# Kernel tuning notes

Measured on AMD Instinct MI355X. Metric: run time of the kernel, lower is better.

The kernel has to match this reference:

```python
import jax, jax.numpy as jnp
import numpy as np

N_NODES = 50000   # num graph nodes
N_EDGES = 800000  # avg degree 16
D = 96            # in_channels == out_channels (residual aggr_out + x)


def setup_inputs() -> dict:
    key = jax.random.key(0)
    k0, k1, k2, k3, k4 = jax.random.split(key, 5)
    x = jax.random.normal(k0, (N_NODES, D), dtype=jnp.float32)
    edge_index = jax.random.randint(k1, (2, N_EDGES), 0, N_NODES)  # [2,E]: row0=src(j), row1=dst(i)
    edge_weight = jax.random.uniform(k2, (N_EDGES,), dtype=jnp.float32)
    pagerank = jax.random.uniform(k3, (N_NODES,), dtype=jnp.float32)
    # nn.Linear(in_channels, out_channels) params
    W = jax.random.normal(k4, (D, D), dtype=jnp.float32) / np.sqrt(D).astype(np.float32)
    b = jnp.zeros((D,), dtype=jnp.float32)
    return {"x": x, "edge_index": edge_index, "edge_weight": edge_weight,
            "pagerank": pagerank, "W": W, "b": b}


def reference(x, edge_index, edge_weight, pagerank, W, b):
    # CGCConv (PyG MessagePassing, aggr='add', flow source_to_target):
    #   message: edge_weight * x_j * pagerank_j   (gather from source nodes)
    #   aggregate: scatter-add to destination nodes
    #   update: Linear(aggr_out + x)
    src = edge_index[0]
    dst = edge_index[1]
    # [E, D] messages: per-edge gather-multiply
    msgs = edge_weight[:, None] * x[src] * pagerank[src][:, None]
    aggr = jax.ops.segment_sum(msgs, dst, num_segments=x.shape[0])  # [N, D]
    return (aggr + x) @ W.T + b
```

## Files before the change

kernel.cpp:

```cpp
#include <hip/hip_runtime.h>


constexpr int NN = 50000;
constexpr int NE = 800000;
constexpr int DD = 96;
constexpr int NB = 196;
constexpr int CAPB = 4608;
constexpr int EPB = 4096;
constexpr int NBLK = (NE + EPB - 1) / EPB;
constexpr int NCVT = (NN * DD / 4 + 511) / 512;

__device__ inline unsigned short f2bf(float f) {
    unsigned u = __float_as_uint(f);
    return (unsigned short)((u + 0x7FFFu + ((u >> 16) & 1u)) >> 16);
}
__device__ inline float bfh(unsigned short v) {
    return __uint_as_float((unsigned)v << 16);
}
__device__ inline unsigned long long pack_e(int meta, float c) {
    return (unsigned long long)(unsigned)meta |
           ((unsigned long long)(unsigned)__float_as_uint(c) << 32);
}

__global__ __launch_bounds__(256) void k_zero(int* __restrict__ cur1) {
    if (threadIdx.x < NB) cur1[threadIdx.x] = 0;
}

__global__ __launch_bounds__(512) void k_prep(const int* __restrict__ src,
                                              const int* __restrict__ dst,
                                              const float* __restrict__ ew,
                                              const float* __restrict__ pr,
                                              int* __restrict__ cur1,
                                              unsigned long long* __restrict__ stage,
                                              const float4* __restrict__ x4,
                                              ushort4* __restrict__ y16v) {
    int tid = threadIdx.x;
    if (blockIdx.x >= NBLK) {
        int i = (blockIdx.x - NBLK) * 512 + tid;
        if (i < NN * DD / 4) {
            float4 v = x4[i];
            y16v[i] = make_ushort4(f2bf(v.x), f2bf(v.y), f2bf(v.z), f2bf(v.w));
        }
        return;
    }
    __shared__ int h[NB];
    __shared__ int gb[NB];
    for (int i = tid; i < NB; i += 512) h[i] = 0;
    __syncthreads();
    int base = blockIdx.x * EPB;

    unsigned long long ent[8]; int bkt[8]; int lrk[8];
    #pragma unroll
    for (int j = 0; j < 8; j++) {
        int e = base + j * 512 + tid;
        bkt[j] = -1;
        if (e < NE) {
            int d = dst[e];
            int s = src[e];
            float c = ew[e] * pr[s];
            bkt[j] = d >> 8;
            lrk[j] = atomicAdd(&h[d >> 8], 1);
            ent[j] = pack_e(s | ((d & 255) << 16), c);
        }
    }
    __syncthreads();
    for (int i = tid; i < NB; i += 512)
        gb[i] = h[i] ? atomicAdd(&cur1[i], h[i]) : 0;
    __syncthreads();
    #pragma unroll
    for (int j = 0; j < 8; j++)
        if (bkt[j] >= 0)
            stage[(size_t)bkt[j] * CAPB + gb[bkt[j]] + lrk[j]] = ent[j];
}

__global__ __launch_bounds__(512) void k_sortB(unsigned long long* __restrict__ stage,
                                               const int* __restrict__ cur1,
                                               int* __restrict__ offs,
                                               int* __restrict__ counts) {
    __shared__ int h[256];
    __shared__ int sc[256];
    __shared__ unsigned long long sorted[CAPB];
    int b = blockIdx.x;
    int tid = threadIdx.x;
    size_t base = (size_t)b * CAPB;
    int n = cur1[b];

    for (int i = tid; i < 256; i += 512) h[i] = 0;
    __syncthreads();

    unsigned long long ent[9]; int lrk[9];
    int m = 0;
    for (int i = tid; i < n; i += 512) {
        unsigned long long e = stage[base + i];
        int dloc = ((int)e >> 16) & 0xff;
        lrk[m] = atomicAdd(&h[dloc], 1);
        ent[m] = e;
        m++;
    }
    __syncthreads();
    if (tid < 256) sc[tid] = h[tid];
    __syncthreads();
    #pragma unroll
    for (int o = 1; o < 256; o <<= 1) {
        int t = 0;
        if (tid < 256 && tid >= o) t = sc[tid - o];
        __syncthreads();
        if (tid < 256) sc[tid] += t;
        __syncthreads();
    }
    m = 0;
    for (int i = tid; i < n; i += 512) {
        unsigned long long e = ent[m];
        int dloc = ((int)e >> 16) & 0xff;
        sorted[sc[dloc] - h[dloc] + lrk[m]] = e;
        m++;
    }
    __syncthreads();
    for (int i = tid; i < n; i += 512) stage[base + i] = sorted[i];
    if (tid < 256) {
        int d = (b << 8) + tid;
        if (d < NN) {
            offs[d] = (int)base + sc[tid] - h[tid];
            counts[d] = h[tid];
        }
    }
}

__global__ __launch_bounds__(256) void k_pull(const ushort4* __restrict__ y16v,
                                              const float4* __restrict__ x4,
                                              const int* __restrict__ offs,
                                              const int* __restrict__ counts,
                                              const unsigned long long* __restrict__ ep,
                                              float4* __restrict__ out4) {
    int g = blockIdx.x * 8 + (threadIdx.x >> 5);
    int lane = threadIdx.x & 31;
    if (g >= NN || lane >= 24) return;
    int beg = offs[g];
    int deg = counts[g];
    float ax = 0.f, ay = 0.f, az = 0.f, aw = 0.f;
    int k = 0;
    for (; k + 8 <= deg; k += 8) {
        unsigned long long e[8];
        #pragma unroll
        for (int j = 0; j < 8; j++) e[j] = ep[beg + k + j];
        ushort4 u[8];
        #pragma unroll
        for (int j = 0; j < 8; j++)
            u[j] = y16v[(size_t)((unsigned)e[j] & 0xffff) * 24 + lane];
        #pragma unroll
        for (int j = 0; j < 8; j++) {
            float c = __uint_as_float((unsigned)(e[j] >> 32));
            ax += c * bfh(u[j].x);
            ay += c * bfh(u[j].y);
            az += c * bfh(u[j].z);
            aw += c * bfh(u[j].w);
        }
    }
    for (; k + 4 <= deg; k += 4) {
        unsigned long long e[4];
        #pragma unroll
        for (int j = 0; j < 4; j++) e[j] = ep[beg + k + j];
        ushort4 u[4];
        #pragma unroll
        for (int j = 0; j < 4; j++)
            u[j] = y16v[(size_t)((unsigned)e[j] & 0xffff) * 24 + lane];
        #pragma unroll
        for (int j = 0; j < 4; j++) {
            float c = __uint_as_float((unsigned)(e[j] >> 32));
            ax += c * bfh(u[j].x);
            ay += c * bfh(u[j].y);
            az += c * bfh(u[j].z);
            aw += c * bfh(u[j].w);
        }
    }
    for (; k < deg; k++) {
        unsigned long long e = ep[beg + k];
        ushort4 u = y16v[(size_t)((unsigned)e & 0xffff) * 24 + lane];
        float c = __uint_as_float((unsigned)(e >> 32));
        ax += c * bfh(u.x);
        ay += c * bfh(u.y);
        az += c * bfh(u.z);
        aw += c * bfh(u.w);
    }
    float4 xn = x4[(size_t)g * 24 + lane];
    out4[(size_t)g * 24 + lane] = make_float4(ax + xn.x, ay + xn.y,
                                              az + xn.z, aw + xn.w);
}

constexpr int SWS = 100;
__global__ __launch_bounds__(256, 4) void k_gemm(float* __restrict__ io,
                                                 const float* __restrict__ W,
                                                 const float* __restrict__ b) {
    __shared__ float sWt[DD * SWS];
    int tid = threadIdx.x;
    for (int i = tid; i < DD * DD; i += 256) {
        int o = i / DD, d = i - o * DD;
        sWt[d * SWS + o] = W[i];
    }
    __syncthreads();

    int wave = tid >> 6, lane = tid & 63;
    int og = lane & 7, rgl = lane >> 3;
    int o0 = og * 12;
    int rbase = blockIdx.x * 128 + wave * 32 + rgl;
    const float4* io4 = (const float4*)io;

    int r[4];
    #pragma unroll
    for (int t = 0; t < 4; t++) {
        int rr = rbase + 8 * t;
        r[t] = (rr < NN) ? rr : (NN - 1);
    }

    float acc[4][12];
    #pragma unroll
    for (int t = 0; t < 4; t++)
        #pragma unroll
        for (int m = 0; m < 12; m++) acc[t][m] = 0.f;

    for (int d4 = 0; d4 < 24; d4++) {
        float4 xv[4];
        #pragma unroll
        for (int t = 0; t < 4; t++) xv[t] = io4[(size_t)r[t] * 24 + d4];
        #pragma unroll
        for (int dj = 0; dj < 4; dj++) {
            const float* wp = &sWt[(d4 * 4 + dj) * SWS + o0];
            float4 w0 = *(const float4*)(wp);
            float4 w1 = *(const float4*)(wp + 4);
            float4 w2 = *(const float4*)(wp + 8);
            #pragma unroll
            for (int t = 0; t < 4; t++) {
                float xs = (dj == 0) ? xv[t].x : (dj == 1) ? xv[t].y
                         : (dj == 2) ? xv[t].z : xv[t].w;
                acc[t][0]  += xs * w0.x;  acc[t][1]  += xs * w0.y;
                acc[t][2]  += xs * w0.z;  acc[t][3]  += xs * w0.w;
                acc[t][4]  += xs * w1.x;  acc[t][5]  += xs * w1.y;
                acc[t][6]  += xs * w1.z;  acc[t][7]  += xs * w1.w;
                acc[t][8]  += xs * w2.x;  acc[t][9]  += xs * w2.y;
                acc[t][10] += xs * w2.z;  acc[t][11] += xs * w2.w;
            }
        }
    }

    float4 b0 = *(const float4*)(b + o0);
    float4 b1 = *(const float4*)(b + o0 + 4);
    float4 b2 = *(const float4*)(b + o0 + 8);
    float4* io4w = (float4*)io;
    #pragma unroll
    for (int t = 0; t < 4; t++) {
        int rr = rbase + 8 * t;
        if (rr < NN) {
            size_t base = (size_t)rr * 24 + og * 3;
            io4w[base + 0] = make_float4(acc[t][0] + b0.x, acc[t][1] + b0.y,
                                         acc[t][2] + b0.z, acc[t][3] + b0.w);
            io4w[base + 1] = make_float4(acc[t][4] + b1.x, acc[t][5] + b1.y,
                                         acc[t][6] + b1.z, acc[t][7] + b1.w);
            io4w[base + 2] = make_float4(acc[t][8] + b2.x, acc[t][9] + b2.y,
                                         acc[t][10] + b2.z, acc[t][11] + b2.w);
        }
    }
}

extern "C" void kernel_launch(void* const* d_in, const int* in_sizes, int n_in,
                              void* d_out, int out_size, void* d_ws, size_t ws_size,
                              hipStream_t stream) {
    const float* x  = (const float*)d_in[0];
    const int*   ei = (const int*)d_in[1];
    const float* ew = (const float*)d_in[2];
    const float* pr = (const float*)d_in[3];
    const float* W  = (const float*)d_in[4];
    const float* b  = (const float*)d_in[5];
    float* out = (float*)d_out;

    unsigned long long* stage = (unsigned long long*)d_ws;
    unsigned short* y16 = (unsigned short*)(stage + (size_t)NB * CAPB);
    int* cur1   = (int*)(y16 + (size_t)NN * DD);
    int* offs   = cur1 + NB;
    int* counts = offs + NN;

    const int* src = ei;
    const int* dst = ei + NE;

    k_zero<<<1, 256, 0, stream>>>(cur1);
    k_prep<<<NBLK + NCVT, 512, 0, stream>>>(src, dst, ew, pr, cur1, stage,
                                            (const float4*)x, (ushort4*)y16);
    k_sortB<<<NB, 512, 0, stream>>>(stage, cur1, offs, counts);
    k_pull<<<(NN + 7) / 8, 256, 0, stream>>>((const ushort4*)y16, (const float4*)x,
                                             offs, counts, stage, (float4*)out);
    k_gemm<<<(NN + 127) / 128, 256, 0, stream>>>(out, W, b);
}
```

Measured before the change: 154.8 us.

## Locally bucket-sort edges before staging and pack edge entries into 32 bits

```diff
diff --git a/kernel.cpp b/kernel.cpp
--- a/kernel.cpp
+++ b/kernel.cpp
@@ -43,11 +43,14 @@
         }
         return;
     }
-    __shared__ int h[NB];
-    __shared__ int gb[NB];
-    for (int i = tid; i < NB; i += 512) h[i] = 0;
+    __shared__ int h[256];
+    __shared__ int gb[256];
+    __shared__ int sc[256];
+    __shared__ unsigned long long sorted[EPB];
+    for (int i = tid; i < 256; i += 512) h[i] = 0;
     __syncthreads();
     int base = blockIdx.x * EPB;
+    int n = min(EPB, NE - base);
 
     unsigned long long ent[8]; int bkt[8]; int lrk[8];
     #pragma unroll
@@ -58,19 +61,36 @@
             int d = dst[e];
             int s = src[e];
             float c = ew[e] * pr[s];
-            bkt[j] = d >> 8;
-            lrk[j] = atomicAdd(&h[d >> 8], 1);
-            ent[j] = pack_e(s | ((d & 255) << 16), c);
-        }
-    }
-    __syncthreads();
+            int bk = d >> 8;
+            bkt[j] = bk;
+            lrk[j] = atomicAdd(&h[bk], 1);
+            ent[j] = pack_e(s | ((d & 255) << 16) | (bk << 24), c);
+        }
+    }
+    __syncthreads();
+    if (tid < 256) sc[tid] = h[tid];
+    __syncthreads();
+    #pragma unroll
+    for (int o = 1; o < 256; o <<= 1) {
+        int t = 0;
+        if (tid < 256 && tid >= o) t = sc[tid - o];
+        __syncthreads();
+        if (tid < 256) sc[tid] += t;
+        __syncthreads();
+    }
     for (int i = tid; i < NB; i += 512)
         gb[i] = h[i] ? atomicAdd(&cur1[i], h[i]) : 0;
     __syncthreads();
     #pragma unroll
     for (int j = 0; j < 8; j++)
         if (bkt[j] >= 0)
-            stage[(size_t)bkt[j] * CAPB + gb[bkt[j]] + lrk[j]] = ent[j];
+            sorted[sc[bkt[j]] - h[bkt[j]] + lrk[j]] = ent[j];
+    __syncthreads();
+    for (int i = tid; i < n; i += 512) {
+        unsigned long long e = sorted[i];
+        int bk = ((int)(e >> 24)) & 0xff;
+        stage[(size_t)bk * CAPB + gb[bk] + (i - (sc[bk] - h[bk]))] = e;
+    }
 }
 
 __global__ __launch_bounds__(512) void k_sortB(unsigned long long* __restrict__ stage,
@@ -79,7 +99,7 @@
                                                int* __restrict__ counts) {
     __shared__ int h[256];
     __shared__ int sc[256];
-    __shared__ unsigned long long sorted[CAPB];
+    __shared__ unsigned sorted[CAPB];
     int b = blockIdx.x;
     int tid = threadIdx.x;
     size_t base = (size_t)b * CAPB;
@@ -88,13 +108,16 @@
     for (int i = tid; i < 256; i += 512) h[i] = 0;
     __syncthreads();
 
-    unsigned long long ent[9]; int lrk[9];
+    unsigned e32[9]; int dl[9]; int lrk[9];
     int m = 0;
     for (int i = tid; i < n; i += 512) {
         unsigned long long e = stage[base + i];
-        int dloc = ((int)e >> 16) & 0xff;
+        int dloc = ((int)(e >> 16)) & 0xff;
+        unsigned cb = (unsigned)(e >> 32);
+        unsigned cbf = (cb + 0x7FFFu + ((cb >> 16) & 1u)) >> 16;
+        e32[m] = ((unsigned)e & 0xffffu) | (cbf << 16);
+        dl[m] = dloc;
         lrk[m] = atomicAdd(&h[dloc], 1);
-        ent[m] = e;
         m++;
     }
     __syncthreads();
@@ -110,17 +133,16 @@
     }
     m = 0;
     for (int i = tid; i < n; i += 512) {
-        unsigned long long e = ent[m];
-        int dloc = ((int)e >> 16) & 0xff;
-        sorted[sc[dloc] - h[dloc] + lrk[m]] = e;
+        sorted[sc[dl[m]] - h[dl[m]] + lrk[m]] = e32[m];
         m++;
     }
     __syncthreads();
-    for (int i = tid; i < n; i += 512) stage[base + i] = sorted[i];
+    unsigned* outp = (unsigned*)(stage + base);
+    for (int i = tid; i < n; i += 512) outp[i] = sorted[i];
     if (tid < 256) {
         int d = (b << 8) + tid;
         if (d < NN) {
-            offs[d] = (int)base + sc[tid] - h[tid];
+            offs[d] = (int)(2 * base) + sc[tid] - h[tid];
             counts[d] = h[tid];
         }
     }
@@ -130,7 +152,7 @@
                                               const float4* __restrict__ x4,
                                               const int* __restrict__ offs,
                                               const int* __restrict__ counts,
-                                              const unsigned long long* __restrict__ ep,
+                                              const unsigned* __restrict__ ep,
                                               float4* __restrict__ out4) {
     int g = blockIdx.x * 8 + (threadIdx.x >> 5);
     int lane = threadIdx.x & 31;
@@ -140,16 +162,16 @@
     float ax = 0.f, ay = 0.f, az = 0.f, aw = 0.f;
     int k = 0;
     for (; k + 8 <= deg; k += 8) {
-        unsigned long long e[8];
+        unsigned e[8];
         #pragma unroll
         for (int j = 0; j < 8; j++) e[j] = ep[beg + k + j];
         ushort4 u[8];
         #pragma unroll
         for (int j = 0; j < 8; j++)
-            u[j] = y16v[(size_t)((unsigned)e[j] & 0xffff) * 24 + lane];
+            u[j] = y16v[(size_t)(e[j] & 0xffff) * 24 + lane];
         #pragma unroll
         for (int j = 0; j < 8; j++) {
-            float c = __uint_as_float((unsigned)(e[j] >> 32));
+            float c = bfh((unsigned short)(e[j] >> 16));
             ax += c * bfh(u[j].x);
             ay += c * bfh(u[j].y);
             az += c * bfh(u[j].z);
@@ -157,16 +179,16 @@
         }
     }
     for (; k + 4 <= deg; k += 4) {
-        unsigned long long e[4];
+        unsigned e[4];
         #pragma unroll
         for (int j = 0; j < 4; j++) e[j] = ep[beg + k + j];
         ushort4 u[4];
         #pragma unroll
         for (int j = 0; j < 4; j++)
-            u[j] = y16v[(size_t)((unsigned)e[j] & 0xffff) * 24 + lane];
+            u[j] = y16v[(size_t)(e[j] & 0xffff) * 24 + lane];
         #pragma unroll
         for (int j = 0; j < 4; j++) {
-            float c = __uint_as_float((unsigned)(e[j] >> 32));
+            float c = bfh((unsigned short)(e[j] >> 16));
             ax += c * bfh(u[j].x);
             ay += c * bfh(u[j].y);
             az += c * bfh(u[j].z);
@@ -174,9 +196,9 @@
         }
     }
     for (; k < deg; k++) {
-        unsigned long long e = ep[beg + k];
-        ushort4 u = y16v[(size_t)((unsigned)e & 0xffff) * 24 + lane];
-        float c = __uint_as_float((unsigned)(e >> 32));
+        unsigned e = ep[beg + k];
+        ushort4 u = y16v[(size_t)(e & 0xffff) * 24 + lane];
+        float c = bfh((unsigned short)(e >> 16));
         ax += c * bfh(u.x);
         ay += c * bfh(u.y);
         az += c * bfh(u.z);
@@ -286,6 +308,7 @@
                                             (const float4*)x, (ushort4*)y16);
     k_sortB<<<NB, 512, 0, stream>>>(stage, cur1, offs, counts);
     k_pull<<<(NN + 7) / 8, 256, 0, stream>>>((const ushort4*)y16, (const float4*)x,
-                                             offs, counts, stage, (float4*)out);
+                                             offs, counts, (const unsigned*)stage,
+                                             (float4*)out);
     k_gemm<<<(NN + 127) / 128, 256, 0, stream>>>(out, W, b);
 }
```

After: 151.0 us. 2.4% less time.
